# Performance work log

Hardware: AMD Instinct MI355X
Metric: run time of the kernel (lower is better)

## Reference

```python
import jax, jax.numpy as jnp
import numpy as np

B, C, H, W = 4, 64, 128, 128
K = 9  # 3x3 kernel taps
OFFSET_SCALE = 1.0
EPS = 1e-5


def conv2d(x, w, b):
    # x: [B,Cin,H,W], w: [Cout,Cin,3,3] -> [B,Cout,H,W] (SAME padding, stride 1)
    out = jax.lax.conv_general_dilated(x, w, (1, 1), 'SAME',
                                       dimension_numbers=('NCHW', 'OIHW', 'NCHW'))
    return out + b[None, :, None, None]


def deform_conv(x, w, b, ow, ob):
    # DCN-style 3x3 deformable conv, stride 1, pad 1, 1 deformable group.
    Bn, Cin, Hh, Ww = x.shape
    off = conv2d(x, ow, ob).reshape(Bn, K, 2, Hh, Ww) * OFFSET_SCALE  # (dy,dx) per tap
    dy = jnp.array([-1, -1, -1, 0, 0, 0, 1, 1, 1], jnp.float32)
    dx = jnp.array([-1, 0, 1, -1, 0, 1, -1, 0, 1], jnp.float32)
    iy = jnp.arange(Hh, dtype=jnp.float32)
    ix = jnp.arange(Ww, dtype=jnp.float32)
    # sampling coords: [B,K,H,W]
    cy = iy[None, None, :, None] + dy[None, :, None, None] + off[:, :, 0]
    cx = ix[None, None, None, :] + dx[None, :, None, None] + off[:, :, 1]
    y0 = jnp.floor(cy); x0 = jnp.floor(cx)
    wy = cy - y0;       wx = cx - x0
    y0i = y0.astype(jnp.int32); x0i = x0.astype(jnp.int32)
    vals = x.reshape(Bn, Cin, Hh * Ww)

    def gather(yi, xi, wgt):
        valid = ((yi >= 0) & (yi < Hh) & (xi >= 0) & (xi < Ww)).astype(x.dtype)
        idx = (jnp.clip(yi, 0, Hh - 1) * Ww + jnp.clip(xi, 0, Ww - 1)).reshape(Bn, 1, K * Hh * Ww)
        g = jnp.take_along_axis(vals, idx, axis=2).reshape(Bn, Cin, K, Hh, Ww)
        return g * (wgt * valid)[:, None]  # zero padding outside image

    samp = (gather(y0i,     x0i,     (1 - wy) * (1 - wx))
          + gather(y0i,     x0i + 1, (1 - wy) * wx)
          + gather(y0i + 1, x0i,     wy * (1 - wx))
          + gather(y0i + 1, x0i + 1, wy * wx))  # [B,Cin,K,H,W]
    out = jnp.einsum('bckhw,ock->bohw', samp, w.reshape(w.shape[0], Cin, K))
    return out + b[None, :, None, None]


def group_norm1(x, gamma, beta):
    # num_groups=1: normalize over (C,H,W) per sample
    m = jnp.mean(x, axis=(1, 2, 3), keepdims=True)
    v = jnp.var(x, axis=(1, 2, 3), keepdims=True)
    return (x - m) * jax.lax.rsqrt(v + EPS) * gamma[None, :, None, None] + beta[None, :, None, None]


def setup_inputs() -> dict:
    key = jax.random.key(0)
    ks = jax.random.split(key, 6)
    n = lambda k, shape, s: jax.random.normal(k, shape, dtype=jnp.float32) * s
    return {
        'x':   jax.random.normal(ks[0], (B, C, H, W), dtype=jnp.float32),
        'w1':  n(ks[1], (C, C, 3, 3), 0.05), 'b1': jnp.zeros((C,), jnp.float32),
        'ow1': n(ks[2], (2 * K, C, 3, 3), 0.01), 'ob1': jnp.zeros((2 * K,), jnp.float32),
        'g1':  jnp.ones((C,), jnp.float32), 'be1': jnp.zeros((C,), jnp.float32),
        'w2':  n(ks[3], (C, C, 3, 3), 0.05), 'b2': jnp.zeros((C,), jnp.float32),
        'ow2': n(ks[4], (2 * K, C, 3, 3), 0.01), 'ob2': jnp.zeros((2 * K,), jnp.float32),
        'g2':  jnp.ones((C,), jnp.float32), 'be2': jnp.zeros((C,), jnp.float32),
    }


def reference(x, w1, b1, ow1, ob1, g1, be1, w2, b2, ow2, ob2, g2, be2):
    # block1: deform_conv -> GN(1) -> relu -> (dropout=identity), + identity shortcut
    h = jax.nn.relu(group_norm1(deform_conv(x, w1, b1, ow1, ob1), g1, be1)) + x
    # block2: same, residual on h
    h = jax.nn.relu(group_norm1(deform_conv(h, w2, b2, ow2, ob2), g2, be2)) + h
    return h
```

## Files before the change

### kernel.cpp

```cpp
#include <hip/hip_runtime.h>
#include <hip/hip_bf16.h>
#include <hip/hip_fp16.h>
#include <math.h>

constexpr int Bz = 4, Cc = 64, Hh = 128, Ww = 128, Kk = 9;
constexpr int HW = Hh * Ww;
constexpr float EPSf = 1e-5f;
constexpr int CK = Cc * Kk;

constexpr int TROWS = 5, TCOLS = 36, TPITCH = 144;

typedef __attribute__((ext_vector_type(8))) short short8;
typedef __attribute__((ext_vector_type(4))) float f32x4;

__device__ __forceinline__ ushort f32_to_bf16(float f) {
    uint u = __float_as_uint(f);
    return (ushort)((u + 0x7fffu + ((u >> 16) & 1u)) >> 16);
}
__device__ __forceinline__ float bf16_to_f32(ushort u) {
    return __uint_as_float((uint)u << 16);
}
__device__ __forceinline__ ushort f32_to_f16b(float f) {
    __half h = __float2half(f);
    return *reinterpret_cast<ushort*>(&h);
}
__device__ __forceinline__ __half2 u32_as_h2(uint u) {
    union { uint u; __half2 h; } c; c.u = u; return c.h;
}
__device__ __forceinline__ uint h2_as_u32(__half2 h) {
    union { uint u; __half2 h; } c; c.h = h; return c.u;
}

__global__ void frag_kernel(const float* __restrict__ w1, const float* __restrict__ w2,
                            const float* __restrict__ ow1, const float* __restrict__ ow2,
                            ushort* __restrict__ wA1, ushort* __restrict__ wA2,
                            ushort* __restrict__ oA1, ushort* __restrict__ oA2) {
    int tid = blockIdx.x * 256 + threadIdx.x;
    if (tid >= 110592) return;
    const float* src; ushort* dst; int e; int cout;
    if (tid < 36864)        { src = w1;  dst = wA1; e = tid;         cout = 64; }
    else if (tid < 73728)   { src = w2;  dst = wA2; e = tid - 36864; cout = 64; }
    else if (tid < 92160)   { src = ow1; dst = oA1; e = tid - 73728; cout = 18; }
    else                    { src = ow2; dst = oA2; e = tid - 92160; cout = 18; }
    int j = e & 7, l = (e >> 3) & 63, kk = (e >> 9) % 18, wo = e / 9216;
    int oc = wo * 16 + (l & 15);
    int kidx = kk * 32 + ((l >> 4) * 8) + j;
    int tap = kidx >> 6, c = kidx & 63;
    dst[e] = (oc < cout) ? f32_to_f16b(src[oc * CK + c * 9 + tap]) : (ushort)0;
}

__global__ __launch_bounds__(256)
void nhwc_kernel(const float* __restrict__ src, ushort* __restrict__ dst) {
    __shared__ float s_t[64][65];
    int blk = blockIdx.x;
    int p0 = (blk & 255) * 64;
    int b = blk >> 8;
    int t = threadIdx.x;
    int tp = t & 63;
    #pragma unroll
    for (int i = 0; i < 16; i++) {
        int c = i * 4 + (t >> 6);
        s_t[c][tp] = src[((size_t)(b * 64 + c)) * HW + p0 + tp];
    }
    __syncthreads();
    #pragma unroll
    for (int i = 0; i < 16; i++) {
        int pl = i * 4 + (t >> 6);
        dst[((size_t)b * HW + p0 + pl) * 64 + tp] = f32_to_f16b(s_t[tp][pl]);
    }
}

__global__ __launch_bounds__(512)
void deform_fused_kernel(const ushort* __restrict__ xnh, const ushort* __restrict__ wA,
                         const ushort* __restrict__ owA, const float* __restrict__ bias,
                         const float* __restrict__ obias, ushort* __restrict__ y,
                         float* __restrict__ part) {
    __shared__ __align__(16) char   s_x[TROWS * TCOLS * TPITCH];
    __shared__ __align__(16) ushort s_a[32 * 584];
    __shared__ __align__(16) uint   s_aw[32 * 9 * 8];
    float (*off_s2)[32][18] = reinterpret_cast<float (*)[32][18]>(s_a);

    int blk = blockIdx.x;
    int wt = blk & 3;
    int h  = (blk >> 2) & 127;
    int b  = blk >> 9;
    int w0 = wt * 32;
    int t = threadIdx.x;
    int wv = t >> 6, lane = t & 63;
    const ushort* xnb = xnh + (size_t)b * HW * 64;
    const char* xnc = reinterpret_cast<const char*>(xnb);

    #pragma unroll
    for (int r = 0; r < 3; r++) {
        int e = r * 512 + t;
        if (e < TROWS * TCOLS * 8) {
            int ch = e & 7, px = e >> 3;
            int row = px / TCOLS, col = px - row * TCOLS;
            int gy = h - 2 + row, gx = w0 - 2 + col;
            uint4 v = {0u, 0u, 0u, 0u};
            if ((unsigned)gy < 128u && (unsigned)gx < 128u)
                v = *reinterpret_cast<const uint4*>(xnc + ((((gy << 7) + gx) << 7) + ch * 16));
            *reinterpret_cast<uint4*>(&s_x[px * TPITCH + ch * 16]) = v;
        }
    }
    __syncthreads();

    {
        int wo = wv & 1, ph = (wv >> 1) & 1, kh = wv >> 2;
        int g = lane >> 4, li = lane & 15;
        int px = ph * 16 + li;
        f32x4 oacc;
        #pragma unroll
        for (int r = 0; r < 4; r++) {
            int oc = wo * 16 + g * 4 + r;
            oacc[r] = (kh == 0 && oc < 18) ? obias[oc] : 0.f;
        }
        const short8* owp = reinterpret_cast<const short8*>(owA) + (wo * 18) * 64 + lane;
        #pragma unroll
        for (int kki = 0; kki < 9; kki++) {
            int kk = kh * 9 + kki;
            int tap = kk >> 1;
            int ky = tap / 3 - 1, kx = tap - (tap / 3) * 3 - 1;
            int cb = (kk & 1) * 64 + g * 16;
            short8 bf = *reinterpret_cast<const short8*>(
                &s_x[((ky + 2) * TCOLS + px + kx + 2) * TPITCH + cb]);
            short8 af = owp[kk * 64];
            oacc = __builtin_amdgcn_mfma_f32_16x16x32_f16(af, bf, oacc, 0, 0, 0);
        }
        #pragma unroll
        for (int r = 0; r < 4; r++) {
            int oc = wo * 16 + g * 4 + r;
            if (oc < 18) off_s2[kh][px][oc] = oacc[r];
        }
    }
    __syncthreads();

    uint aw_l[8];
    bool has_unit = (t < 288);
    if (has_unit) {
        int px = t / 9, k = t - px * 9;
        int ky = k / 3 - 1, kx = k - (k / 3) * 3 - 1;
        float ody = off_s2[0][px][2 * k]     + off_s2[1][px][2 * k];
        float odx = off_s2[0][px][2 * k + 1] + off_s2[1][px][2 * k + 1];
        float cy = (float)(h + ky) + ody;
        float cx = (float)(w0 + px + kx) + odx;
        float fy = floorf(cy), fx = floorf(cx);
        float wy = cy - fy, wx = cx - fx;
        int y0 = (int)fy, x0 = (int)fx;
        int y1 = y0 + 1, x1 = x0 + 1;
        bool vy0 = (unsigned)y0 < 128u, vy1 = (unsigned)y1 < 128u;
        bool vx0 = (unsigned)x0 < 128u, vx1 = (unsigned)x1 < 128u;
        int yc0 = min(max(y0, 0), 127), yc1 = min(max(y1, 0), 127);
        int xc0 = min(max(x0, 0), 127), xc1 = min(max(x1, 0), 127);
        int r0 = yc0 - (h - 2),  r1 = yc1 - (h - 2);
        int c0t = xc0 - (w0 - 2), c1t = xc1 - (w0 - 2);
        bool intile = ((unsigned)r0 < (unsigned)TROWS) && ((unsigned)r1 < (unsigned)TROWS)
                   && ((unsigned)c0t < (unsigned)TCOLS) && ((unsigned)c1t < (unsigned)TCOLS);
        uint a00, a01, a10, a11;
        if (intile) {
            a00 = (uint)((r0 * TCOLS + c0t) * TPITCH);
            a01 = (uint)((r0 * TCOLS + c1t) * TPITCH);
            a10 = (uint)((r1 * TCOLS + c0t) * TPITCH);
            a11 = (uint)((r1 * TCOLS + c1t) * TPITCH);
        } else {
            a00 = (uint)(((yc0 << 7) + xc0) << 7) | 0x80000000u;
            a01 = (uint)(((yc0 << 7) + xc1) << 7) | 0x80000000u;
            a10 = (uint)(((yc1 << 7) + xc0) << 7) | 0x80000000u;
            a11 = (uint)(((yc1 << 7) + xc1) << 7) | 0x80000000u;
        }
        aw_l[0] = a00; aw_l[1] = __float_as_uint((vy0 && vx0) ? (1.f - wy) * (1.f - wx) : 0.f);
        aw_l[2] = a01; aw_l[3] = __float_as_uint((vy0 && vx1) ? (1.f - wy) * wx : 0.f);
        aw_l[4] = a10; aw_l[5] = __float_as_uint((vy1 && vx0) ? wy * (1.f - wx) : 0.f);
        aw_l[6] = a11; aw_l[7] = __float_as_uint((vy1 && vx1) ? wy * wx : 0.f);
    }
    __syncthreads();
    if (has_unit) {
        uint base = (uint)t * 8;
        #pragma unroll
        for (int i = 0; i < 8; i++) s_aw[base + i] = aw_l[i];
    }
    __syncthreads();

    {
        int sub = lane >> 3;
        int ci  = lane & 7;
        int co  = ci << 4;
        char* s_ab = reinterpret_cast<char*>(s_a);
        #pragma unroll
        for (int i = 0; i < 5; i++) {
            int lu = i * 8 + sub;
            if (lu < 36) {
                int U = wv * 36 + lu;
                int px = U / 9;
                int tap = U - px * 9;
                uint4 q0 = *reinterpret_cast<const uint4*>(&s_aw[U * 8]);
                uint4 q1 = *reinterpret_cast<const uint4*>(&s_aw[U * 8 + 4]);
                uint4 v00, v01, v10, v11;
                if (!(q0.x & 0x80000000u)) {
                    v00 = *reinterpret_cast<const uint4*>(&s_x[q0.x + co]);
                    v01 = *reinterpret_cast<const uint4*>(&s_x[q0.z + co]);
                    v10 = *reinterpret_cast<const uint4*>(&s_x[q1.x + co]);
                    v11 = *reinterpret_cast<const uint4*>(&s_x[q1.z + co]);
                } else {
                    v00 = *reinterpret_cast<const uint4*>(xnc + ((q0.x & 0x7fffffffu) + co));
                    v01 = *reinterpret_cast<const uint4*>(xnc + ((q0.z & 0x7fffffffu) + co));
                    v10 = *reinterpret_cast<const uint4*>(xnc + ((q1.x & 0x7fffffffu) + co));
                    v11 = *reinterpret_cast<const uint4*>(xnc + ((q1.z & 0x7fffffffu) + co));
                }
                __half2 W00 = __float2half2_rn(__uint_as_float(q0.y));
                __half2 W01 = __float2half2_rn(__uint_as_float(q0.w));
                __half2 W10 = __float2half2_rn(__uint_as_float(q1.y));
                __half2 W11 = __float2half2_rn(__uint_as_float(q1.w));
                __half2 r0 = __hmul2(W00, u32_as_h2(v00.x));
                __half2 r1 = __hmul2(W00, u32_as_h2(v00.y));
                __half2 r2 = __hmul2(W00, u32_as_h2(v00.z));
                __half2 r3 = __hmul2(W00, u32_as_h2(v00.w));
                r0 = __hfma2(W01, u32_as_h2(v01.x), r0);
                r1 = __hfma2(W01, u32_as_h2(v01.y), r1);
                r2 = __hfma2(W01, u32_as_h2(v01.z), r2);
                r3 = __hfma2(W01, u32_as_h2(v01.w), r3);
                r0 = __hfma2(W10, u32_as_h2(v10.x), r0);
                r1 = __hfma2(W10, u32_as_h2(v10.y), r1);
                r2 = __hfma2(W10, u32_as_h2(v10.z), r2);
                r3 = __hfma2(W10, u32_as_h2(v10.w), r3);
                r0 = __hfma2(W11, u32_as_h2(v11.x), r0);
                r1 = __hfma2(W11, u32_as_h2(v11.y), r1);
                r2 = __hfma2(W11, u32_as_h2(v11.z), r2);
                r3 = __hfma2(W11, u32_as_h2(v11.w), r3);
                uint4 outv;
                outv.x = h2_as_u32(r0);
                outv.y = h2_as_u32(r1);
                outv.z = h2_as_u32(r2);
                outv.w = h2_as_u32(r3);
                *reinterpret_cast<uint4*>(s_ab + px * 1168 + tap * 128 + co) = outv;
            }
        }
    }
    __syncthreads();

    int wo = wv & 3, ph = wv >> 2;
    int g = lane >> 4, li = lane & 15;
    f32x4 acc;
    const float* bp = bias + wo * 16 + g * 4;
    acc.x = bp[0]; acc.y = bp[1]; acc.z = bp[2]; acc.w = bp[3];
    const short8* ap = reinterpret_cast<const short8*>(wA) + (wo * 18) * 64 + lane;
    const ushort* sp = s_a + (ph * 16 + li) * 584 + g * 8;
    #pragma unroll
    for (int kk = 0; kk < 18; kk++) {
        short8 af = ap[kk * 64];
        short8 bf = *reinterpret_cast<const short8*>(sp + kk * 32);
        acc = __builtin_amdgcn_mfma_f32_16x16x32_f16(af, bf, acc, 0, 0, 0);
    }
    size_t ybase = ((size_t)(b * 64 + wo * 16 + g * 4)) * HW + h * Ww + w0 + ph * 16 + li;
    y[ybase]           = f32_to_bf16(acc.x);
    y[ybase + HW]      = f32_to_bf16(acc.y);
    y[ybase + 2 * HW]  = f32_to_bf16(acc.z);
    y[ybase + 3 * HW]  = f32_to_bf16(acc.w);

    float s  = acc.x + acc.y + acc.z + acc.w;
    float s2 = acc.x * acc.x + acc.y * acc.y + acc.z * acc.z + acc.w * acc.w;
    #pragma unroll
    for (int o = 32; o > 0; o >>= 1) {
        s  += __shfl_down(s, o);
        s2 += __shfl_down(s2, o);
    }
    float* redbuf = reinterpret_cast<float*>(s_aw);
    if (lane == 0) { redbuf[wv * 2] = s; redbuf[wv * 2 + 1] = s2; }
    __syncthreads();
    if (t == 0) {
        float a = 0.f, c2 = 0.f;
        #pragma unroll
        for (int i = 0; i < 8; i++) { a += redbuf[i * 2]; c2 += redbuf[i * 2 + 1]; }
        part[blk * 2]     = a;
        part[blk * 2 + 1] = c2;
    }
}

__global__ void gn_stats_kernel(const float* __restrict__ part, float* __restrict__ stats) {
    __shared__ float ls[4][2];
    int b = blockIdx.x;
    int t = threadIdx.x;
    int i0 = (b * 512 + t) * 2, i1 = (b * 512 + 256 + t) * 2;
    float s  = part[i0]     + part[i1];
    float s2 = part[i0 + 1] + part[i1 + 1];
    #pragma unroll
    for (int o = 32; o > 0; o >>= 1) {
        s  += __shfl_down(s, o);
        s2 += __shfl_down(s2, o);
    }
    int wave = t >> 6, lane = t & 63;
    if (lane == 0) { ls[wave][0] = s; ls[wave][1] = s2; }
    __syncthreads();
    if (t == 0) {
        float a = 0.f, c = 0.f;
        #pragma unroll
        for (int i = 0; i < 4; i++) { a += ls[i][0]; c += ls[i][1]; }
        const float n = (float)(Cc * HW);
        float m = a / n;
        float var = c / n - m * m;
        stats[b * 2]     = m;
        stats[b * 2 + 1] = rsqrtf(var + EPSf);
    }
}

__global__ __launch_bounds__(256)
void gn_fin1_kernel(const ushort* __restrict__ y, const float* __restrict__ res,
                    const float* __restrict__ g, const float* __restrict__ be,
                    const float* __restrict__ stats, ushort* __restrict__ h1bf,
                    ushort* __restrict__ hnh) {
    __shared__ float s_t[64][65];
    int blk = blockIdx.x;
    int p0 = (blk & 255) * 64;
    int b = blk >> 8;
    int t = threadIdx.x;
    int tp = t & 63;
    float m = stats[b * 2], rs = stats[b * 2 + 1];
    #pragma unroll
    for (int i = 0; i < 16; i++) {
        int c = i * 4 + (t >> 6);
        size_t idx = ((size_t)(b * 64 + c)) * HW + p0 + tp;
        float v = (bf16_to_f32(y[idx]) - m) * rs * g[c] + be[c];
        v = fmaxf(v, 0.f) + res[idx];
        h1bf[idx] = f32_to_bf16(v);
        s_t[c][tp] = v;
    }
    __syncthreads();
    #pragma unroll
    for (int i = 0; i < 16; i++) {
        int pl = i * 4 + (t >> 6);
        hnh[((size_t)b * HW + p0 + pl) * 64 + tp] = f32_to_f16b(s_t[tp][pl]);
    }
}

__global__ __launch_bounds__(256)
void gn_fin2_kernel(const ushort* __restrict__ y, const ushort* __restrict__ resbf,
                    const float* __restrict__ g, const float* __restrict__ be,
                    const float* __restrict__ stats, float* __restrict__ out) {
    int idx = (blockIdx.x * 256 + threadIdx.x) * 4;
    int c = (idx >> 14) & 63;
    int b = idx >> 20;
    float m = stats[b * 2], rs = stats[b * 2 + 1];
    float gc = g[c], bc = be[c];
    ushort4 yv = *reinterpret_cast<const ushort4*>(y + idx);
    ushort4 rv = *reinterpret_cast<const ushort4*>(resbf + idx);
    float4 o;
    o.x = fmaxf((bf16_to_f32(yv.x) - m) * rs * gc + bc, 0.f) + bf16_to_f32(rv.x);
    o.y = fmaxf((bf16_to_f32(yv.y) - m) * rs * gc + bc, 0.f) + bf16_to_f32(rv.y);
    o.z = fmaxf((bf16_to_f32(yv.z) - m) * rs * gc + bc, 0.f) + bf16_to_f32(rv.z);
    o.w = fmaxf((bf16_to_f32(yv.w) - m) * rs * gc + bc, 0.f) + bf16_to_f32(rv.w);
    *reinterpret_cast<float4*>(out + idx) = o;
}

extern "C" void kernel_launch(void* const* d_in, const int* in_sizes, int n_in,
                              void* d_out, int out_size, void* d_ws, size_t ws_size,
                              hipStream_t stream) {
    const float* x   = (const float*)d_in[0];
    const float* w1  = (const float*)d_in[1];
    const float* b1  = (const float*)d_in[2];
    const float* ow1 = (const float*)d_in[3];
    const float* ob1 = (const float*)d_in[4];
    const float* g1  = (const float*)d_in[5];
    const float* be1 = (const float*)d_in[6];
    const float* w2  = (const float*)d_in[7];
    const float* b2  = (const float*)d_in[8];
    const float* ow2 = (const float*)d_in[9];
    const float* ob2 = (const float*)d_in[10];
    const float* g2  = (const float*)d_in[11];
    const float* be2 = (const float*)d_in[12];
    float* out = (float*)d_out;

    ushort* ybuf = (ushort*)d_ws;
    ushort* h1bf = ybuf + (size_t)Bz * Cc * HW;
    ushort* xnh  = h1bf + (size_t)Bz * Cc * HW;
    ushort* hnh  = xnh + (size_t)Bz * HW * 64;
    ushort* wA1  = hnh + (size_t)Bz * HW * 64;
    ushort* wA2  = wA1 + 36864;
    ushort* owA1 = wA2 + 36864;
    ushort* owA2 = owA1 + 18432;
    float* part  = (float*)(owA2 + 18432);
    float* stats = part + 4096;

    frag_kernel<<<(110592 + 255) / 256, 256, 0, stream>>>(w1, w2, ow1, ow2, wA1, wA2, owA1, owA2);
    nhwc_kernel<<<Bz * (HW / 64), 256, 0, stream>>>(x, xnh);

    deform_fused_kernel<<<Bz * Hh * (Ww / 32), 512, 0, stream>>>(xnh, wA1, owA1, b1, ob1, ybuf, part);
    gn_stats_kernel<<<Bz, 256, 0, stream>>>(part, stats);
    gn_fin1_kernel<<<Bz * (HW / 64), 256, 0, stream>>>(ybuf, x, g1, be1, stats, h1bf, hnh);

    deform_fused_kernel<<<Bz * Hh * (Ww / 32), 512, 0, stream>>>(hnh, wA2, owA2, b2, ob2, ybuf, part);
    gn_stats_kernel<<<Bz, 256, 0, stream>>>(part, stats);
    gn_fin2_kernel<<<Bz * Cc * HW / 1024, 256, 0, stream>>>(ybuf, h1bf, g2, be2, stats, out);
}
```

Before: 100.3 us.

## Drop shared input tile and make offset/coord stages wave-local without block barriers

Removes the block-wide staging of the input halo tile in shared memory. Each wave now computes the offset conv for its own 16 pixels directly from global memory, covering all 18 offset channels. The sampling coordinates are then computed and consumed within the same wave, which eliminates three __syncthreads and the tile-load phase. The bilinear gathers now always read from global/L1 instead of LDS. The cost is redundant offset-conv MFMA work and global loads across waves, plus more cache traffic for the gathers.

Result: slower. 180.1 us (+79.6%).

```diff
diff --git a/kernel.cpp b/kernel.cpp
--- a/kernel.cpp
+++ b/kernel.cpp
@@ -7,8 +7,6 @@
 constexpr int HW = Hh * Ww;
 constexpr float EPSf = 1e-5f;
 constexpr int CK = Cc * Kk;
-
-constexpr int TROWS = 5, TCOLS = 36, TPITCH = 144;
 
 typedef __attribute__((ext_vector_type(8))) short short8;
 typedef __attribute__((ext_vector_type(4))) float f32x4;
@@ -75,10 +73,9 @@
                          const ushort* __restrict__ owA, const float* __restrict__ bias,
                          const float* __restrict__ obias, ushort* __restrict__ y,
                          float* __restrict__ part) {
-    __shared__ __align__(16) char   s_x[TROWS * TCOLS * TPITCH];
     __shared__ __align__(16) ushort s_a[32 * 584];
-    __shared__ __align__(16) uint   s_aw[32 * 9 * 8];
-    float (*off_s2)[32][18] = reinterpret_cast<float (*)[32][18]>(s_a);
+    __shared__ float s_offw[8][16 * 18];
+    __shared__ __align__(16) uint  s_awc[8][36][4];
 
     int blk = blockIdx.x;
     int wt = blk & 3;
@@ -87,99 +84,57 @@
     int w0 = wt * 32;
     int t = threadIdx.x;
     int wv = t >> 6, lane = t & 63;
+    int g = lane >> 4, li = lane & 15;
+    int ph = wv >> 2;
     const ushort* xnb = xnh + (size_t)b * HW * 64;
     const char* xnc = reinterpret_cast<const char*>(xnb);
 
-    #pragma unroll
-    for (int r = 0; r < 3; r++) {
-        int e = r * 512 + t;
-        if (e < TROWS * TCOLS * 8) {
-            int ch = e & 7, px = e >> 3;
-            int row = px / TCOLS, col = px - row * TCOLS;
-            int gy = h - 2 + row, gx = w0 - 2 + col;
-            uint4 v = {0u, 0u, 0u, 0u};
-            if ((unsigned)gy < 128u && (unsigned)gx < 128u)
-                v = *reinterpret_cast<const uint4*>(xnc + ((((gy << 7) + gx) << 7) + ch * 16));
-            *reinterpret_cast<uint4*>(&s_x[px * TPITCH + ch * 16]) = v;
+    {
+        f32x4 oa0, oa1;
+        #pragma unroll
+        for (int r = 0; r < 4; r++) {
+            oa0[r] = obias[g * 4 + r];
+            oa1[r] = (g == 0 && r < 2) ? obias[16 + r] : 0.f;
         }
-    }
-    __syncthreads();
-
-    {
-        int wo = wv & 1, ph = (wv >> 1) & 1, kh = wv >> 2;
-        int g = lane >> 4, li = lane & 15;
-        int px = ph * 16 + li;
-        f32x4 oacc;
-        #pragma unroll
-        for (int r = 0; r < 4; r++) {
-            int oc = wo * 16 + g * 4 + r;
-            oacc[r] = (kh == 0 && oc < 18) ? obias[oc] : 0.f;
-        }
-        const short8* owp = reinterpret_cast<const short8*>(owA) + (wo * 18) * 64 + lane;
-        #pragma unroll
-        for (int kki = 0; kki < 9; kki++) {
-            int kk = kh * 9 + kki;
+        const short8* owf = reinterpret_cast<const short8*>(owA) + lane;
+        #pragma unroll
+        for (int kk = 0; kk < 18; kk++) {
             int tap = kk >> 1;
             int ky = tap / 3 - 1, kx = tap - (tap / 3) * 3 - 1;
             int cb = (kk & 1) * 64 + g * 16;
-            short8 bf = *reinterpret_cast<const short8*>(
-                &s_x[((ky + 2) * TCOLS + px + kx + 2) * TPITCH + cb]);
-            short8 af = owp[kk * 64];
-            oacc = __builtin_amdgcn_mfma_f32_16x16x32_f16(af, bf, oacc, 0, 0, 0);
+            int gy = h + ky, gx = w0 + ph * 16 + li + kx;
+            bool valid = ((unsigned)gy < 128u) && ((unsigned)gx < 128u);
+            short8 bf = {0, 0, 0, 0, 0, 0, 0, 0};
+            if (valid)
+                bf = *reinterpret_cast<const short8*>(xnc + ((((gy << 7) + gx) << 7) + cb));
+            oa0 = __builtin_amdgcn_mfma_f32_16x16x32_f16(owf[(0 * 18 + kk) * 64], bf, oa0, 0, 0, 0);
+            oa1 = __builtin_amdgcn_mfma_f32_16x16x32_f16(owf[(1 * 18 + kk) * 64], bf, oa1, 0, 0, 0);
         }
         #pragma unroll
-        for (int r = 0; r < 4; r++) {
-            int oc = wo * 16 + g * 4 + r;
-            if (oc < 18) off_s2[kh][px][oc] = oacc[r];
+        for (int r = 0; r < 4; r++)
+            s_offw[wv][li * 18 + g * 4 + r] = oa0[r];
+        if (g == 0) {
+            s_offw[wv][li * 18 + 16] = oa1[0];
+            s_offw[wv][li * 18 + 17] = oa1[1];
         }
     }
-    __syncthreads();
-
-    uint aw_l[8];
-    bool has_unit = (t < 288);
-    if (has_unit) {
-        int px = t / 9, k = t - px * 9;
+
+    if (lane < 36) {
+        int u = lane;
+        int pxl = u / 9, k = u - pxl * 9;
+        int px = (wv << 2) + pxl;
+        int phloc = px & 15;
         int ky = k / 3 - 1, kx = k - (k / 3) * 3 - 1;
-        float ody = off_s2[0][px][2 * k]     + off_s2[1][px][2 * k];
-        float odx = off_s2[0][px][2 * k + 1] + off_s2[1][px][2 * k + 1];
+        float ody = s_offw[wv][phloc * 18 + 2 * k];
+        float odx = s_offw[wv][phloc * 18 + 2 * k + 1];
         float cy = (float)(h + ky) + ody;
         float cx = (float)(w0 + px + kx) + odx;
         float fy = floorf(cy), fx = floorf(cx);
-        float wy = cy - fy, wx = cx - fx;
         int y0 = (int)fy, x0 = (int)fx;
-        int y1 = y0 + 1, x1 = x0 + 1;
-        bool vy0 = (unsigned)y0 < 128u, vy1 = (unsigned)y1 < 128u;
-        bool vx0 = (unsigned)x0 < 128u, vx1 = (unsigned)x1 < 128u;
-        int yc0 = min(max(y0, 0), 127), yc1 = min(max(y1, 0), 127);
-        int xc0 = min(max(x0, 0), 127), xc1 = min(max(x1, 0), 127);
-        int r0 = yc0 - (h - 2),  r1 = yc1 - (h - 2);
-        int c0t = xc0 - (w0 - 2), c1t = xc1 - (w0 - 2);
-        bool intile = ((unsigned)r0 < (unsigned)TROWS) && ((unsigned)r1 < (unsigned)TROWS)
-                   && ((unsigned)c0t < (unsigned)TCOLS) && ((unsigned)c1t < (unsigned)TCOLS);
-        uint a00, a01, a10, a11;
-        if (intile) {
-            a00 = (uint)((r0 * TCOLS + c0t) * TPITCH);
-            a01 = (uint)((r0 * TCOLS + c1t) * TPITCH);
-            a10 = (uint)((r1 * TCOLS + c0t) * TPITCH);
-            a11 = (uint)((r1 * TCOLS + c1t) * TPITCH);
-        } else {
-            a00 = (uint)(((yc0 << 7) + xc0) << 7) | 0x80000000u;
-            a01 = (uint)(((yc0 << 7) + xc1) << 7) | 0x80000000u;
-            a10 = (uint)(((yc1 << 7) + xc0) << 7) | 0x80000000u;
-            a11 = (uint)(((yc1 << 7) + xc1) << 7) | 0x80000000u;
-        }
-        aw_l[0] = a00; aw_l[1] = __float_as_uint((vy0 && vx0) ? (1.f - wy) * (1.f - wx) : 0.f);
-        aw_l[2] = a01; aw_l[3] = __float_as_uint((vy0 && vx1) ? (1.f - wy) * wx : 0.f);
-        aw_l[4] = a10; aw_l[5] = __float_as_uint((vy1 && vx0) ? wy * (1.f - wx) : 0.f);
-        aw_l[6] = a11; aw_l[7] = __float_as_uint((vy1 && vx1) ? wy * wx : 0.f);
-    }
-    __syncthreads();
-    if (has_unit) {
-        uint base = (uint)t * 8;
-        #pragma unroll
-        for (int i = 0; i < 8; i++) s_aw[base + i] = aw_l[i];
-    }
-    __syncthreads();
+        s_awc[wv][u][0] = (uint)(y0 & 0xffff) | ((uint)x0 << 16);
+        s_awc[wv][u][1] = __float_as_uint(cy - fy);
+        s_awc[wv][u][2] = __float_as_uint(cx - fx);
+    }
 
     {
         int sub = lane >> 3;
@@ -190,27 +145,34 @@
         for (int i = 0; i < 5; i++) {
             int lu = i * 8 + sub;
             if (lu < 36) {
-                int U = wv * 36 + lu;
-                int px = U / 9;
-                int tap = U - px * 9;
-                uint4 q0 = *reinterpret_cast<const uint4*>(&s_aw[U * 8]);
-                uint4 q1 = *reinterpret_cast<const uint4*>(&s_aw[U * 8 + 4]);
-                uint4 v00, v01, v10, v11;
-                if (!(q0.x & 0x80000000u)) {
-                    v00 = *reinterpret_cast<const uint4*>(&s_x[q0.x + co]);
-                    v01 = *reinterpret_cast<const uint4*>(&s_x[q0.z + co]);
-                    v10 = *reinterpret_cast<const uint4*>(&s_x[q1.x + co]);
-                    v11 = *reinterpret_cast<const uint4*>(&s_x[q1.z + co]);
-                } else {
-                    v00 = *reinterpret_cast<const uint4*>(xnc + ((q0.x & 0x7fffffffu) + co));
-                    v01 = *reinterpret_cast<const uint4*>(xnc + ((q0.z & 0x7fffffffu) + co));
-                    v10 = *reinterpret_cast<const uint4*>(xnc + ((q1.x & 0x7fffffffu) + co));
-                    v11 = *reinterpret_cast<const uint4*>(xnc + ((q1.z & 0x7fffffffu) + co));
-                }
-                __half2 W00 = __float2half2_rn(__uint_as_float(q0.y));
-                __half2 W01 = __float2half2_rn(__uint_as_float(q0.w));
-                __half2 W10 = __float2half2_rn(__uint_as_float(q1.y));
-                __half2 W11 = __float2half2_rn(__uint_as_float(q1.w));
+                int pxl = lu / 9, tap = lu - pxl * 9;
+                int px = (wv << 2) + pxl;
+                uint yx = s_awc[wv][lu][0];
+                float wy = __uint_as_float(s_awc[wv][lu][1]);
+                float wx = __uint_as_float(s_awc[wv][lu][2]);
+                int y0 = (short)(yx & 0xffffu);
+                int x0 = (short)(yx >> 16);
+                int y1 = y0 + 1, x1 = x0 + 1;
+                bool vy0 = (unsigned)y0 < 128u, vy1 = (unsigned)y1 < 128u;
+                bool vx0 = (unsigned)x0 < 128u, vx1 = (unsigned)x1 < 128u;
+                int yc0 = min(max(y0, 0), 127), yc1 = min(max(y1, 0), 127);
+                int xc0 = min(max(x0, 0), 127), xc1 = min(max(x1, 0), 127);
+                uint a00 = (uint)(((yc0 << 7) + xc0) << 7) + co;
+                uint a01 = (uint)(((yc0 << 7) + xc1) << 7) + co;
+                uint a10 = (uint)(((yc1 << 7) + xc0) << 7) + co;
+                uint a11 = (uint)(((yc1 << 7) + xc1) << 7) + co;
+                float w00 = (vy0 && vx0) ? (1.f - wy) * (1.f - wx) : 0.f;
+                float w01 = (vy0 && vx1) ? (1.f - wy) * wx : 0.f;
+                float w10 = (vy1 && vx0) ? wy * (1.f - wx) : 0.f;
+                float w11 = (vy1 && vx1) ? wy * wx : 0.f;
+                uint4 v00 = *reinterpret_cast<const uint4*>(xnc + a00);
+                uint4 v01 = *reinterpret_cast<const uint4*>(xnc + a01);
+                uint4 v10 = *reinterpret_cast<const uint4*>(xnc + a10);
+                uint4 v11 = *reinterpret_cast<const uint4*>(xnc + a11);
+                __half2 W00 = __float2half2_rn(w00);
+                __half2 W01 = __float2half2_rn(w01);
+                __half2 W10 = __float2half2_rn(w10);
+                __half2 W11 = __float2half2_rn(w11);
                 __half2 r0 = __hmul2(W00, u32_as_h2(v00.x));
                 __half2 r1 = __hmul2(W00, u32_as_h2(v00.y));
                 __half2 r2 = __hmul2(W00, u32_as_h2(v00.z));
@@ -238,20 +200,19 @@
     }
     __syncthreads();
 
-    int wo = wv & 3, ph = wv >> 2;
-    int g = lane >> 4, li = lane & 15;
+    int wo = wv & 3, ph2 = wv >> 2;
     f32x4 acc;
     const float* bp = bias + wo * 16 + g * 4;
     acc.x = bp[0]; acc.y = bp[1]; acc.z = bp[2]; acc.w = bp[3];
     const short8* ap = reinterpret_cast<const short8*>(wA) + (wo * 18) * 64 + lane;
-    const ushort* sp = s_a + (ph * 16 + li) * 584 + g * 8;
+    const ushort* sp = s_a + (ph2 * 16 + li) * 584 + g * 8;
     #pragma unroll
     for (int kk = 0; kk < 18; kk++) {
         short8 af = ap[kk * 64];
         short8 bf = *reinterpret_cast<const short8*>(sp + kk * 32);
         acc = __builtin_amdgcn_mfma_f32_16x16x32_f16(af, bf, acc, 0, 0, 0);
     }
-    size_t ybase = ((size_t)(b * 64 + wo * 16 + g * 4)) * HW + h * Ww + w0 + ph * 16 + li;
+    size_t ybase = ((size_t)(b * 64 + wo * 16 + g * 4)) * HW + h * Ww + w0 + ph2 * 16 + li;
     y[ybase]           = f32_to_bf16(acc.x);
     y[ybase + HW]      = f32_to_bf16(acc.y);
     y[ybase + 2 * HW]  = f32_to_bf16(acc.z);
@@ -264,7 +225,7 @@
         s  += __shfl_down(s, o);
         s2 += __shfl_down(s2, o);
     }
-    float* redbuf = reinterpret_cast<float*>(s_aw);
+    float* redbuf = reinterpret_cast<float*>(s_awc);
     if (lane == 0) { redbuf[wv * 2] = s; redbuf[wv * 2 + 1] = s2; }
     __syncthreads();
     if (t == 0) {
```
